# Optimization experiments

Measured on AMD Instinct MI355X. Metric: run time of the kernel, lower is better.

## Reference

```python
import jax, jax.numpy as jnp
import numpy as np

B, D_IN, NF = 8192, 64, 128
D1 = 1 + D_IN              # 65  : first linear input (bias col + x)
O1 = 1 + NF                # 129 : o width after first layer
IN2 = O1 + NF * NF         # 16513 : polylayer-1 input width
O2 = O1 + NF               # 257
IN3 = O2 + NF * NF         # 16641 : polylayer-2 input width
FC_IN = 1 + 3 * NF + 3 * NF  # 769 : cat(o, og) width


def setup_inputs() -> dict:
    key = jax.random.key(0)
    ks = jax.random.split(key, 16)
    w = lambda k, shape: jax.random.normal(k, shape, jnp.float32) * 0.02
    return {
        "x": jax.random.normal(ks[0], (B, D_IN), jnp.float32),
        "bias0": jnp.asarray(1.0, jnp.float32),
        "Wf1": w(ks[1], (D1, NF)), "bf1": w(ks[2], (NF,)),
        "Wg1": w(ks[3], (D1, NF)), "bg1": w(ks[4], (NF,)),
        "Wf2": w(ks[5], (IN2, NF)), "bf2": w(ks[6], (NF,)),
        "Wg2": w(ks[7], (IN2, NF)), "bg2": w(ks[8], (NF,)),
        "Wf3": w(ks[9], (IN3, NF)), "bf3": w(ks[10], (NF,)),
        "Wg3": w(ks[11], (IN3, NF)), "bg3": w(ks[12], (NF,)),
        "Wfc": w(ks[13], (FC_IN, 1)), "bfc": w(ks[14], (1,)),
    }


def reference(x, bias0, Wf1, bf1, Wg1, bg1, Wf2, bf2, Wg2, bg2,
              Wf3, bf3, Wg3, bg3, Wfc, bfc):
    Bn = x.shape[0]
    o = jnp.ones((Bn, 1), x.dtype) * bias0          # bias column
    z = jnp.concatenate([o, x], axis=1)              # [B, 1+D_in]
    og = z @ Wg1 + bg1                               # vanishing branch
    ot = z @ Wf1 + bf1                               # nonvanishing branch
    o1 = ot                                          # degree-1 features, kept fixed
    o = jnp.concatenate([o, ot], axis=1)
    for Wf, bf, Wg, bg in ((Wf2, bf2, Wg2, bg2), (Wf3, bf3, Wg3, bg3)):
        # batched outer product o1_i ot_i^T, row-major flatten -> [B, nf1*nf_t]
        outer = (o1[:, :, None] * ot[:, None, :]).reshape(Bn, -1)
        xx = jnp.concatenate([o, outer], axis=1)
        xf = xx @ Wf + bf
        xg = xx @ Wg + bg
        ot = xf
        o = jnp.concatenate([o, xf], axis=1)
        og = jnp.concatenate([og, xg], axis=1)
    return jnp.concatenate([o, og], axis=1) @ Wfc + bfc
```

## Files before the change

### kernel.cpp

```cpp
#include <hip/hip_runtime.h>

typedef _Float16 f16;
typedef _Float16 f16x8 __attribute__((ext_vector_type(8)));
typedef float f32x4 __attribute__((ext_vector_type(4)));

static constexpr size_t PART_STRIDE = (size_t)8192 * 256;

static constexpr size_t OFF_W2   = 0;
static constexpr size_t SZ_W2    = (size_t)516 * 8192 * 2;
static constexpr size_t OFF_W3   = OFF_W2 + SZ_W2;
static constexpr size_t SZ_W3    = (size_t)520 * 8192 * 2;
static constexpr size_t OFF_OT1  = OFF_W3 + SZ_W3;
static constexpr size_t OFF_XF2  = OFF_OT1 + (size_t)8192 * 128 * 2;
static constexpr size_t OFF_C2   = OFF_XF2 + (size_t)8192 * 128 * 2;
static constexpr size_t OFF_C3   = OFF_C2 + 1024;
static constexpr size_t OFF_ACC  = OFF_C3 + 1024;
static constexpr size_t OFF_PART = OFF_ACC + 32768;

template<int LAYER>
__device__ __forceinline__
void prep_w_body(int t, const float* __restrict__ Wf, const float* __restrict__ Wg,
                 f16* __restrict__ Wswz)
{
    const int s = t >> 10, rem = t & 1023;
    const int nt = rem >> 6, l = rem & 63;
    const int n = nt * 16 + (l & 15);
    const int klb = (l >> 4) * 8;
    f16x8 o;
#pragma unroll
    for (int e = 0; e < 8; ++e) {
        const int kl = klb + e;
        int row;
        if (LAYER == 2) {
            if (s < 4) row = 1 + s * 32 + kl;
            else { const int u = s - 4; row = 129 + (u & 127) * 128 + (u >> 7) * 32 + kl; }
        } else {
            if (s < 8) row = 1 + s * 32 + kl;
            else { const int u = s - 8; row = 257 + (u & 127) * 128 + (u >> 7) * 32 + kl; }
        }
        const float v = (n < 128) ? Wf[(size_t)row * 128 + n]
                                  : Wg[(size_t)row * 128 + (n - 128)];
        o[e] = (f16)v;
    }
    *(f16x8*)(Wswz + (size_t)t * 8) = o;
}

__global__ __launch_bounds__(256)
void prep_fused(const float* __restrict__ x, const float* __restrict__ bias0,
                const float* __restrict__ Wf1, const float* __restrict__ bf1,
                const float* __restrict__ Wg1, const float* __restrict__ bg1,
                const float* __restrict__ Wf2, const float* __restrict__ bf2,
                const float* __restrict__ Wg2, const float* __restrict__ bg2,
                const float* __restrict__ Wf3, const float* __restrict__ bf3,
                const float* __restrict__ Wg3, const float* __restrict__ bg3,
                const float* __restrict__ Wfc, const float* __restrict__ bfc,
                f16* __restrict__ W2s, f16* __restrict__ W3s,
                float* __restrict__ c2, float* __restrict__ c3,
                f16* __restrict__ ot1f16, float* __restrict__ outacc)
{
    const int bid = blockIdx.x;
    __shared__ float wp[4];
    if (bid < 2064) {
        prep_w_body<2>(bid * 256 + threadIdx.x, Wf2, Wg2, W2s);
    } else if (bid < 4144) {
        prep_w_body<3>((bid - 2064) * 256 + threadIdx.x, Wf3, Wg3, W3s);
    } else if (bid == 4144) {
        const int n = threadIdx.x;
        const float b0 = bias0[0];
        if (n < 128) { c2[n] = bf2[n] + b0 * Wf2[n]; c3[n] = bf3[n] + b0 * Wf3[n]; }
        else { const int m = n - 128; c2[n] = bg2[m] + b0 * Wg2[m]; c3[n] = bg3[m] + b0 * Wg3[m]; }
    } else {
        const int half = threadIdx.x >> 7;
        const int n = threadIdx.x & 127;
        const int r = (bid - 4145) * 2 + half;
        const float b0 = bias0[0];
        float sf = b0 * Wf1[n] + bf1[n];
        float sg = b0 * Wg1[n] + bg1[n];
        const float* xr = x + (size_t)r * 64;
#pragma unroll 8
        for (int k = 0; k < 64; ++k) {
            const float xv = xr[k];
            sf = fmaf(xv, Wf1[(k + 1) * 128 + n], sf);
            sg = fmaf(xv, Wg1[(k + 1) * 128 + n], sg);
        }
        ot1f16[(size_t)r * 128 + n] = (f16)sf;
        float p = sf * Wfc[1 + n] + sg * Wfc[385 + n];
#pragma unroll
        for (int off = 32; off; off >>= 1) p += __shfl_down(p, off);
        if ((threadIdx.x & 63) == 0) wp[threadIdx.x >> 6] = p;
        __syncthreads();
        if ((threadIdx.x & 127) == 0)
            outacc[r] = bfc[0] + b0 * Wfc[0] + wp[half * 2] + wp[half * 2 + 1];
    }
}


#define STAGE(S_W, BUF) do {                                                        \
    const f16* _src = wsrc0 + (size_t)(S_W) * 8192;                                 \
    __builtin_amdgcn_global_load_lds(                                               \
        (const __attribute__((address_space(1))) unsigned int*)_src,                \
        (__attribute__((address_space(3))) unsigned int*)&wring[BUF][tid * 8],      \
        16, 0, 0);                                                                  \
} while (0)

#define WAITVX(N) asm volatile("s_waitcnt vmcnt(" #N ") lgkmcnt(0)" ::: "memory")
#define WAITV(N) WAITVX(N)

#define RSTEP(O1CUR, O1NXT, I8, E, WN, LN)                                          \
{                                                                                   \
    const int s_ = (I8) * 8 + (E);                                                  \
    WAITV(WN);                                                                      \
    __builtin_amdgcn_s_barrier();                                                   \
    __builtin_amdgcn_sched_barrier(0);                                              \
    {                                                                               \
        const int sn_ = (s_ + 2 < 128) ? s_ + 2 : 127;           \
        STAGE(out_base + sn_, (s_ + 2) % 3);                                        \
    }                                                                               \
    if ((LN) && (E) == 0) {                                                         \
        _Pragma("unroll")                                                           \
        for (int mi = 0; mi < 8; ++mi)                                              \
            O1NXT[mi] = *(const f16x8*)(ot1_row + mi * 2048 + ((I8) + 1) * 8);      \
    }                                                                               \
    const f16* wb_ = &wring[s_ % 3][0];                                             \
    const f16x8 b0_ = *(const f16x8*)(wb_ + (wc * 128 + lane) * 8);                 \
    const f16x8 b1_ = *(const f16x8*)(wb_ + (wc * 128 + 64 + lane) * 8);            \
    _Pragma("unroll")                                                               \
    for (int mi = 0; mi < 8; ++mi) {                                                \
        const f16x8 a_ = featreg[mi] * O1CUR[mi][E];                                \
        acc[mi][0] = __builtin_amdgcn_mfma_f32_16x16x32_f16(a_, b0_, acc[mi][0], 0, 0, 0); \
        acc[mi][1] = __builtin_amdgcn_mfma_f32_16x16x32_f16(a_, b1_, acc[mi][1], 0, 0, 0); \
    }                                                                               \
}

#define RBODY(O1CUR, O1NXT, I8, W1, LN)     \
    RSTEP(O1CUR, O1NXT, I8, 0, 1, LN)       \
    RSTEP(O1CUR, O1NXT, I8, 1, W1, LN)      \
    RSTEP(O1CUR, O1NXT, I8, 2, 1, LN)       \
    RSTEP(O1CUR, O1NXT, I8, 3, 1, LN)       \
    RSTEP(O1CUR, O1NXT, I8, 4, 1, LN)       \
    RSTEP(O1CUR, O1NXT, I8, 5, 1, LN)       \
    RSTEP(O1CUR, O1NXT, I8, 6, 1, LN)       \
    RSTEP(O1CUR, O1NXT, I8, 7, 1, LN)

template<int LAYER>
__global__ __launch_bounds__(256, 2)
void gemm_poly(const f16* __restrict__ Wswz, const f16* featg,
               const f16* ot1g, float* __restrict__ partials)
{
    __shared__ f16 wring[3][2048];

    constexpr int NLIN = (LAYER == 2) ? 4 : 8;
    constexpr int CLIN = (LAYER == 2) ? 1 : 2;

    const int bid = blockIdx.x;
    const int rb = bid >> 4;
    const int sp = (bid >> 2) & 3;
    const int nb = bid & 3;
    const int r0 = rb * 256;
    const int tid = threadIdx.x;
    const int wid = tid >> 6, lane = tid & 63;
    const int wr = wid >> 1, wc = wid & 1;
    const int lhi = lane >> 4, llo = lane & 15;

    const f16* wsrc0 = Wswz + nb * 2048 + tid * 8;
    const f16* ot1_row  = ot1g  + (size_t)(r0 + wr * 128 + llo) * 128;
    const f16* feat_row = featg + (size_t)(r0 + wr * 128 + llo) * 128;

    f32x4 acc[8][2] = {};
    const int out_base = NLIN + sp * 128;

    f16x8 featreg[8], o1A[8], o1B[8];
#pragma unroll
    for (int mi = 0; mi < 8; ++mi) {
        featreg[mi] = *(const f16x8*)(feat_row + mi * 2048 + sp * 32 + lhi * 8);
        o1A[mi]     = *(const f16x8*)(ot1_row + mi * 2048);
    }

    STAGE(CLIN * sp, 0);
    __syncthreads();
#pragma unroll
    for (int c = 0; c < CLIN; ++c) {
        if (c + 1 < CLIN) STAGE(CLIN * sp + c + 1, 1);
        const int s = CLIN * sp + c;
        const int col = s * 32 + lhi * 8;
        const f16* wb = &wring[c][0];
        const f16x8 b0 = *(const f16x8*)(wb + (wc * 128 + lane) * 8);
        const f16x8 b1 = *(const f16x8*)(wb + (wc * 128 + 64 + lane) * 8);
#pragma unroll
        for (int mi = 0; mi < 8; ++mi) {
            f16x8 a;
            if (LAYER == 2) a = *(const f16x8*)(ot1_row + mi * 2048 + col);
            else a = (col < 128) ? *(const f16x8*)(ot1_row + mi * 2048 + col)
                                 : *(const f16x8*)(feat_row + mi * 2048 + (col - 128));
            acc[mi][0] = __builtin_amdgcn_mfma_f32_16x16x32_f16(a, b0, acc[mi][0], 0, 0, 0);
            acc[mi][1] = __builtin_amdgcn_mfma_f32_16x16x32_f16(a, b1, acc[mi][1], 0, 0, 0);
        }
        __syncthreads();
    }

    STAGE(out_base + 0, 0);
    STAGE(out_base + 1, 1);

    for (int i8 = 0; i8 < 14; i8 += 2) {
        RBODY(o1A, o1B, i8,     9, 1)
        RBODY(o1B, o1A, i8 + 1, 9, 1)
    }
    RBODY(o1A, o1B, 14, 9, 1)
    RBODY(o1B, o1A, 15, 1, 0)

    float* pout = partials + (size_t)sp * PART_STRIDE
                + (size_t)(r0 + wr * 128) * 256 + nb * 64 + wc * 32 + llo;
#pragma unroll
    for (int mi = 0; mi < 8; ++mi)
#pragma unroll
        for (int ni = 0; ni < 2; ++ni)
#pragma unroll
            for (int q = 0; q < 4; ++q)
                pout[(size_t)(mi * 16 + lhi * 4 + q) * 256 + ni * 16] = acc[mi][ni][q];
}

#undef RBODY
#undef RSTEP
#undef WAITV
#undef WAITVX
#undef STAGE

template<int LAYER>
__global__ __launch_bounds__(256)
void reduce_poly(const float* __restrict__ partials, const float* __restrict__ cvec,
                 const float* __restrict__ Wfc, f16* __restrict__ xf_out,
                 float* __restrict__ outacc, float* __restrict__ outp)
{
    const int r = blockIdx.x;
    const int n = threadIdx.x;
    const size_t idx = (size_t)r * 256 + n;
    float v = partials[idx] + partials[idx + PART_STRIDE]
            + partials[idx + 2 * PART_STRIDE] + partials[idx + 3 * PART_STRIDE];
    v += cvec[n];
    if (LAYER == 2 && n < 128)
        xf_out[(size_t)r * 128 + n] = (f16)v;
    const int wseg = (LAYER == 2) ? (n < 128 ? 129 + n : 513 + (n - 128))
                                  : (n < 128 ? 257 + n : 641 + (n - 128));
    float p = v * Wfc[wseg];
#pragma unroll
    for (int off = 32; off; off >>= 1) p += __shfl_down(p, off);
    __shared__ float wp[4];
    if ((threadIdx.x & 63) == 0) wp[threadIdx.x >> 6] = p;
    __syncthreads();
    if (threadIdx.x == 0) {
        const float tot = wp[0] + wp[1] + wp[2] + wp[3];
        if (LAYER == 2) outacc[r] += tot;
        else            outp[r] = outacc[r] + tot;
    }
}

extern "C" void kernel_launch(void* const* d_in, const int* in_sizes, int n_in,
                              void* d_out, int out_size, void* d_ws, size_t ws_size,
                              hipStream_t stream)
{
    (void)in_sizes; (void)n_in; (void)out_size; (void)ws_size;
    const float* x     = (const float*)d_in[0];
    const float* bias0 = (const float*)d_in[1];
    const float* Wf1   = (const float*)d_in[2];
    const float* bf1   = (const float*)d_in[3];
    const float* Wg1   = (const float*)d_in[4];
    const float* bg1   = (const float*)d_in[5];
    const float* Wf2   = (const float*)d_in[6];
    const float* bf2   = (const float*)d_in[7];
    const float* Wg2   = (const float*)d_in[8];
    const float* bg2   = (const float*)d_in[9];
    const float* Wf3   = (const float*)d_in[10];
    const float* bf3   = (const float*)d_in[11];
    const float* Wg3   = (const float*)d_in[12];
    const float* bg3   = (const float*)d_in[13];
    const float* Wfc   = (const float*)d_in[14];
    const float* bfc   = (const float*)d_in[15];
    float* out = (float*)d_out;

    char* ws = (char*)d_ws;
    f16*   W2s    = (f16*)(ws + OFF_W2);
    f16*   W3s    = (f16*)(ws + OFF_W3);
    f16*   ot1f16 = (f16*)(ws + OFF_OT1);
    f16*   xf2f16 = (f16*)(ws + OFF_XF2);
    float* c2     = (float*)(ws + OFF_C2);
    float* c3     = (float*)(ws + OFF_C3);
    float* outacc = (float*)(ws + OFF_ACC);
    float* parts  = (float*)(ws + OFF_PART);

    prep_fused<<<8241, 256, 0, stream>>>(x, bias0, Wf1, bf1, Wg1, bg1,
                                         Wf2, bf2, Wg2, bg2, Wf3, bf3, Wg3, bg3,
                                         Wfc, bfc, W2s, W3s, c2, c3, ot1f16, outacc);
    gemm_poly<2><<<512, 256, 0, stream>>>(W2s, ot1f16, ot1f16, parts);
    reduce_poly<2><<<8192, 256, 0, stream>>>(parts, c2, Wfc, xf2f16, outacc, out);
    gemm_poly<3><<<512, 256, 0, stream>>>(W3s, xf2f16, ot1f16, parts);
    reduce_poly<3><<<8192, 256, 0, stream>>>(parts, c3, Wfc, nullptr, outacc, out);
}
```

Baseline: 295.9 us.

## Deepen weight ring to four stages and register-prefetch B fragments

```diff
diff --git a/kernel.cpp b/kernel.cpp
--- a/kernel.cpp
+++ b/kernel.cpp
@@ -106,48 +106,50 @@
 #define WAITVX(N) asm volatile("s_waitcnt vmcnt(" #N ") lgkmcnt(0)" ::: "memory")
 #define WAITV(N) WAITVX(N)
 
-#define RSTEP(O1CUR, O1NXT, I8, E, WN, LN)                                          \
+#define RSTEP(O1CUR, O1NXT, BCUR, BNXT, I8, E, WN, LN)                              \
 {                                                                                   \
     const int s_ = (I8) * 8 + (E);                                                  \
     WAITV(WN);                                                                      \
     __builtin_amdgcn_s_barrier();                                                   \
     __builtin_amdgcn_sched_barrier(0);                                              \
-    {                                                                               \
-        const int sn_ = (s_ + 2 < 128) ? s_ + 2 : 127;           \
-        STAGE(out_base + sn_, (s_ + 2) % 3);                                        \
+    {                                  \
+        const f16* wb_ = &wring[(s_ + 1) & 3][0];                                   \
+        BNXT[0] = *(const f16x8*)(wb_ + (wc * 128 + lane) * 8);                     \
+        BNXT[1] = *(const f16x8*)(wb_ + (wc * 128 + 64 + lane) * 8);                \
     }                                                                               \
+    __builtin_amdgcn_s_setprio(1);                                                  \
+    _Pragma("unroll")                                                               \
+    for (int mi = 0; mi < 8; ++mi) {                                                \
+        const f16x8 a_ = featreg[mi] * O1CUR[mi][E];                                \
+        acc[mi][0] = __builtin_amdgcn_mfma_f32_16x16x32_f16(a_, BCUR[0], acc[mi][0], 0, 0, 0); \
+        acc[mi][1] = __builtin_amdgcn_mfma_f32_16x16x32_f16(a_, BCUR[1], acc[mi][1], 0, 0, 0); \
+    }                                                                               \
+    __builtin_amdgcn_s_setprio(0);                                                  \
+    {   const int sn_ = (s_ + 3 < 128) ? s_ + 3 : 127;           \
+        STAGE(out_base + sn_, (s_ + 3) & 3); }                                      \
     if ((LN) && (E) == 0) {                                                         \
         _Pragma("unroll")                                                           \
         for (int mi = 0; mi < 8; ++mi)                                              \
             O1NXT[mi] = *(const f16x8*)(ot1_row + mi * 2048 + ((I8) + 1) * 8);      \
     }                                                                               \
-    const f16* wb_ = &wring[s_ % 3][0];                                             \
-    const f16x8 b0_ = *(const f16x8*)(wb_ + (wc * 128 + lane) * 8);                 \
-    const f16x8 b1_ = *(const f16x8*)(wb_ + (wc * 128 + 64 + lane) * 8);            \
-    _Pragma("unroll")                                                               \
-    for (int mi = 0; mi < 8; ++mi) {                                                \
-        const f16x8 a_ = featreg[mi] * O1CUR[mi][E];                                \
-        acc[mi][0] = __builtin_amdgcn_mfma_f32_16x16x32_f16(a_, b0_, acc[mi][0], 0, 0, 0); \
-        acc[mi][1] = __builtin_amdgcn_mfma_f32_16x16x32_f16(a_, b1_, acc[mi][1], 0, 0, 0); \
-    }                                                                               \
-}
-
-#define RBODY(O1CUR, O1NXT, I8, W1, LN)     \
-    RSTEP(O1CUR, O1NXT, I8, 0, 1, LN)       \
-    RSTEP(O1CUR, O1NXT, I8, 1, W1, LN)      \
-    RSTEP(O1CUR, O1NXT, I8, 2, 1, LN)       \
-    RSTEP(O1CUR, O1NXT, I8, 3, 1, LN)       \
-    RSTEP(O1CUR, O1NXT, I8, 4, 1, LN)       \
-    RSTEP(O1CUR, O1NXT, I8, 5, 1, LN)       \
-    RSTEP(O1CUR, O1NXT, I8, 6, 1, LN)       \
-    RSTEP(O1CUR, O1NXT, I8, 7, 1, LN)
+}
+
+#define RBODY(O1CUR, O1NXT, I8, W1, LN)             \
+    RSTEP(O1CUR, O1NXT, bP, bQ, I8, 0, 1, LN)       \
+    RSTEP(O1CUR, O1NXT, bQ, bP, I8, 1, W1, LN)      \
+    RSTEP(O1CUR, O1NXT, bP, bQ, I8, 2, 1, LN)       \
+    RSTEP(O1CUR, O1NXT, bQ, bP, I8, 3, 1, LN)       \
+    RSTEP(O1CUR, O1NXT, bP, bQ, I8, 4, 1, LN)       \
+    RSTEP(O1CUR, O1NXT, bQ, bP, I8, 5, 1, LN)       \
+    RSTEP(O1CUR, O1NXT, bP, bQ, I8, 6, 1, LN)       \
+    RSTEP(O1CUR, O1NXT, bQ, bP, I8, 7, 1, LN)
 
 template<int LAYER>
 __global__ __launch_bounds__(256, 2)
 void gemm_poly(const f16* __restrict__ Wswz, const f16* featg,
                const f16* ot1g, float* __restrict__ partials)
 {
-    __shared__ f16 wring[3][2048];
+    __shared__ f16 wring[4][2048];
 
     constexpr int NLIN = (LAYER == 2) ? 4 : 8;
     constexpr int CLIN = (LAYER == 2) ? 1 : 2;
@@ -200,6 +202,16 @@
 
     STAGE(out_base + 0, 0);
     STAGE(out_base + 1, 1);
+    STAGE(out_base + 2, 2);
+    WAITV(2);
+    __builtin_amdgcn_s_barrier();
+    __builtin_amdgcn_sched_barrier(0);
+    f16x8 bP[2], bQ[2];
+    {
+        const f16* wb = &wring[0][0];
+        bP[0] = *(const f16x8*)(wb + (wc * 128 + lane) * 8);
+        bP[1] = *(const f16x8*)(wb + (wc * 128 + 64 + lane) * 8);
+    }
 
     for (int i8 = 0; i8 < 14; i8 += 2) {
         RBODY(o1A, o1B, i8,     9, 1)
```

Measured after the change: 295.4 us. Within noise of the previous version (-0.2%).
